# Optimization experiments

Measured on AMD Instinct MI355X. Metric: run time of the kernel, lower is better.

## Reference

```python
import jax, jax.numpy as jnp
import numpy as np

N_NODES = 50000
N_EDGES = 1600000
IN_DIM = 128
HID = 64   # per-head hidden/out dim
HEADS = 2
NEG_SLOPE = 0.2


def _gat_layer(x, src, dst, W, attn_l, attn_r, bias):
    # x: [N, Fin]; W: [Fin, H*D]; attn_l/attn_r: [H, D]; bias: [H, D]
    N = x.shape[0]
    H, D = attn_l.shape
    feat = (x @ W).reshape(N, H, D)                      # [N,H,D]
    el = jnp.sum(feat * attn_l, axis=-1)                 # [N,H]
    er = jnp.sum(feat * attn_r, axis=-1)                 # [N,H]
    e = jax.nn.leaky_relu(el[src] + er[dst], NEG_SLOPE)  # [E,H]
    # segment softmax over destination nodes
    m = jax.ops.segment_max(e, dst, num_segments=N)      # [N,H]
    ex = jnp.exp(e - m[dst])                             # [E,H]
    s = jax.ops.segment_sum(ex, dst, num_segments=N)     # [N,H]
    alpha = ex / s[dst]                                  # [E,H]
    msg = feat[src] * alpha[..., None]                   # [E,H,D]
    out = jax.ops.segment_sum(msg, dst, num_segments=N)  # [N,H,D]
    out = out + bias                                     # per-head bias
    # encoder: mean over heads, then ELU
    return jax.nn.elu(out.mean(axis=1))                  # [N,D]


def setup_inputs() -> dict:
    key = jax.random.key(0)
    ks = jax.random.split(key, 12)
    features = jax.random.normal(ks[0], (N_NODES, IN_DIM), dtype=jnp.float32)
    src = jax.random.randint(ks[1], (N_EDGES,), 0, N_NODES, dtype=jnp.int32)
    dst = jax.random.randint(ks[2], (N_EDGES,), 0, N_NODES, dtype=jnp.int32)
    sc1 = 1.0 / np.sqrt(IN_DIM)
    sc2 = 1.0 / np.sqrt(HID)
    W1 = jax.random.normal(ks[3], (IN_DIM, HEADS * HID), dtype=jnp.float32) * sc1
    al1 = jax.random.normal(ks[4], (HEADS, HID), dtype=jnp.float32) * sc2
    ar1 = jax.random.normal(ks[5], (HEADS, HID), dtype=jnp.float32) * sc2
    b1 = jnp.zeros((HEADS, HID), dtype=jnp.float32)
    W2 = jax.random.normal(ks[6], (HID, HEADS * HID), dtype=jnp.float32) * sc2
    al2 = jax.random.normal(ks[7], (HEADS, HID), dtype=jnp.float32) * sc2
    ar2 = jax.random.normal(ks[8], (HEADS, HID), dtype=jnp.float32) * sc2
    b2 = jnp.zeros((HEADS, HID), dtype=jnp.float32)
    return {"features": features, "W1": W1, "al1": al1, "ar1": ar1, "b1": b1,
            "W2": W2, "al2": al2, "ar2": ar2, "b2": b2, "src": src, "dst": dst}


def reference(features, W1, al1, ar1, b1, W2, al2, ar2, b2, src, dst):
    h = _gat_layer(features, src, dst, W1, al1, ar1, b1)  # [N, HID]
    h = _gat_layer(h, src, dst, W2, al2, ar2, b2)         # [N, HID]
    return h
```

## Files before the change

### kernel.cpp

```cpp
#include <hip/hip_runtime.h>
#include <hip/hip_fp16.h>
#include <math.h>

#define N_NODES 50000
#define N_EDGES 1600000
#define SLOTS 96
#define NODES_PER_GRP 6250
#define FILL_BLOCKS 832
#define GEMM1_BLOCKS ((N_NODES + 31) / 32)

typedef int v4i __attribute__((ext_vector_type(4)));


__global__ __launch_bounds__(256) void fused_fill_gemm1(
    const int* __restrict__ src, const int* __restrict__ dst,
    int* __restrict__ cursor, int* __restrict__ ssrc,
    const float* __restrict__ x,
    const float* __restrict__ W,
    const float* __restrict__ al,
    const float* __restrict__ ar,
    __half* __restrict__ feat,
    float* __restrict__ el,
    float* __restrict__ er) {
    constexpr int K = 128;
    constexpr int LDX = K + 4;
    __shared__ float xs[32 * LDX];

    if (blockIdx.x < FILL_BLOCKS) {
        const int g = blockIdx.x & 7;
        const int bg = blockIdx.x >> 3;
        const int nbg = FILL_BLOCKS >> 3;
        const int lo = g * NODES_PER_GRP;
        const int hi = lo + NODES_PER_GRP;
        const v4i* d4 = (const v4i*)dst;
        const v4i* s4 = (const v4i*)src;
        const int E4 = N_EDGES >> 2;

        for (int i = bg * 256 + threadIdx.x; i < E4; i += nbg * 256) {
            v4i d = __builtin_nontemporal_load(d4 + i);
            v4i s = __builtin_nontemporal_load(s4 + i);
            if (d.x >= lo && d.x < hi) {
                int p = atomicAdd(&cursor[d.x], 1);
                if (p < SLOTS) ssrc[d.x * SLOTS + p] = s.x;
            }
            if (d.y >= lo && d.y < hi) {
                int p = atomicAdd(&cursor[d.y], 1);
                if (p < SLOTS) ssrc[d.y * SLOTS + p] = s.y;
            }
            if (d.z >= lo && d.z < hi) {
                int p = atomicAdd(&cursor[d.z], 1);
                if (p < SLOTS) ssrc[d.z * SLOTS + p] = s.z;
            }
            if (d.w >= lo && d.w < hi) {
                int p = atomicAdd(&cursor[d.w], 1);
                if (p < SLOTS) ssrc[d.w * SLOTS + p] = s.w;
            }
        }
        return;
    }

    const int tid = threadIdx.x;
    const int node0 = (blockIdx.x - FILL_BLOCKS) * 32;
    const int N = N_NODES;

    for (int i = tid; i < 32 * K / 4; i += 256) {
        int r = i / (K / 4), c4 = i % (K / 4);
        float4 v = make_float4(0.f, 0.f, 0.f, 0.f);
        if (node0 + r < N) v = *(const float4*)&x[(size_t)(node0 + r) * K + c4 * 4];
        *(float4*)&xs[r * LDX + c4 * 4] = v;
    }
    __syncthreads();

    const int tx = tid & 31;
    const int ty = tid >> 5;
    const int col = tx * 4;

    float acc[4][4];
#pragma unroll
    for (int r = 0; r < 4; ++r)
#pragma unroll
        for (int c = 0; c < 4; ++c) acc[r][c] = 0.f;

    for (int kb = 0; kb < K / 4; ++kb) {
        float4 w0 = *(const float4*)&W[(kb * 4 + 0) * 128 + col];
        float4 w1 = *(const float4*)&W[(kb * 4 + 1) * 128 + col];
        float4 w2 = *(const float4*)&W[(kb * 4 + 2) * 128 + col];
        float4 w3 = *(const float4*)&W[(kb * 4 + 3) * 128 + col];
        float4 xv[4];
#pragma unroll
        for (int r = 0; r < 4; ++r)
            xv[r] = *(const float4*)&xs[(ty * 4 + r) * LDX + kb * 4];
#pragma unroll
        for (int r = 0; r < 4; ++r) {
            acc[r][0] += xv[r].x * w0.x + xv[r].y * w1.x + xv[r].z * w2.x + xv[r].w * w3.x;
            acc[r][1] += xv[r].x * w0.y + xv[r].y * w1.y + xv[r].z * w2.y + xv[r].w * w3.y;
            acc[r][2] += xv[r].x * w0.z + xv[r].y * w1.z + xv[r].z * w2.z + xv[r].w * w3.z;
            acc[r][3] += xv[r].x * w0.w + xv[r].y * w1.w + xv[r].z * w2.w + xv[r].w * w3.w;
        }
    }

    float4 alv = *(const float4*)&al[col];
    float4 arv = *(const float4*)&ar[col];
    float elp[4], erp[4];
#pragma unroll
    for (int r = 0; r < 4; ++r) {
        int n = node0 + ty * 4 + r;
        float4 f = make_float4(acc[r][0], acc[r][1], acc[r][2], acc[r][3]);
        if (n < N) {
            __half2 p0 = __floats2half2_rn(f.x, f.y);
            __half2 p1 = __floats2half2_rn(f.z, f.w);
            union { __half2 h2[2]; uint2 u; } pk;
            pk.h2[0] = p0; pk.h2[1] = p1;
            *(uint2*)&feat[(size_t)n * 128 + col] = pk.u;
        }
        elp[r] = f.x * alv.x + f.y * alv.y + f.z * alv.z + f.w * alv.w;
        erp[r] = f.x * arv.x + f.y * arv.y + f.z * arv.z + f.w * arv.w;
    }
#pragma unroll
    for (int m = 1; m <= 8; m <<= 1) {
#pragma unroll
        for (int r = 0; r < 4; ++r) {
            elp[r] += __shfl_xor(elp[r], m, 64);
            erp[r] += __shfl_xor(erp[r], m, 64);
        }
    }
    int h = tx >> 4;
    if ((tx & 15) == 0) {
#pragma unroll
        for (int r = 0; r < 4; ++r) {
            int n = node0 + ty * 4 + r;
            if (n < N) {
                el[n * 2 + h] = elp[r];
                er[n * 2 + h] = erp[r];
            }
        }
    }
}


template <int K>
__global__ __launch_bounds__(256) void gemm_elr_kernel(
    const float* __restrict__ x, const float* __restrict__ W,
    const float* __restrict__ al, const float* __restrict__ ar,
    __half* __restrict__ feat, float* __restrict__ el, float* __restrict__ er,
    int N) {
    constexpr int LDX = K + 4;
    __shared__ float xs[32 * LDX];
    const int tid = threadIdx.x;
    const int node0 = blockIdx.x * 32;

    for (int i = tid; i < 32 * K / 4; i += 256) {
        int r = i / (K / 4), c4 = i % (K / 4);
        float4 v = make_float4(0.f, 0.f, 0.f, 0.f);
        if (node0 + r < N) v = *(const float4*)&x[(size_t)(node0 + r) * K + c4 * 4];
        *(float4*)&xs[r * LDX + c4 * 4] = v;
    }
    __syncthreads();

    const int tx = tid & 31;
    const int ty = tid >> 5;
    const int col = tx * 4;

    float acc[4][4];
#pragma unroll
    for (int r = 0; r < 4; ++r)
#pragma unroll
        for (int c = 0; c < 4; ++c) acc[r][c] = 0.f;

    for (int kb = 0; kb < K / 4; ++kb) {
        float4 w0 = *(const float4*)&W[(kb * 4 + 0) * 128 + col];
        float4 w1 = *(const float4*)&W[(kb * 4 + 1) * 128 + col];
        float4 w2 = *(const float4*)&W[(kb * 4 + 2) * 128 + col];
        float4 w3 = *(const float4*)&W[(kb * 4 + 3) * 128 + col];
        float4 xv[4];
#pragma unroll
        for (int r = 0; r < 4; ++r)
            xv[r] = *(const float4*)&xs[(ty * 4 + r) * LDX + kb * 4];
#pragma unroll
        for (int r = 0; r < 4; ++r) {
            acc[r][0] += xv[r].x * w0.x + xv[r].y * w1.x + xv[r].z * w2.x + xv[r].w * w3.x;
            acc[r][1] += xv[r].x * w0.y + xv[r].y * w1.y + xv[r].z * w2.y + xv[r].w * w3.y;
            acc[r][2] += xv[r].x * w0.z + xv[r].y * w1.z + xv[r].z * w2.z + xv[r].w * w3.z;
            acc[r][3] += xv[r].x * w0.w + xv[r].y * w1.w + xv[r].z * w2.w + xv[r].w * w3.w;
        }
    }

    float4 alv = *(const float4*)&al[col];
    float4 arv = *(const float4*)&ar[col];
    float elp[4], erp[4];
#pragma unroll
    for (int r = 0; r < 4; ++r) {
        int n = node0 + ty * 4 + r;
        float4 f = make_float4(acc[r][0], acc[r][1], acc[r][2], acc[r][3]);
        if (n < N) {
            __half2 p0 = __floats2half2_rn(f.x, f.y);
            __half2 p1 = __floats2half2_rn(f.z, f.w);
            union { __half2 h2[2]; uint2 u; } pk;
            pk.h2[0] = p0; pk.h2[1] = p1;
            *(uint2*)&feat[(size_t)n * 128 + col] = pk.u;
        }
        elp[r] = f.x * alv.x + f.y * alv.y + f.z * alv.z + f.w * alv.w;
        erp[r] = f.x * arv.x + f.y * arv.y + f.z * arv.z + f.w * arv.w;
    }
#pragma unroll
    for (int m = 1; m <= 8; m <<= 1) {
#pragma unroll
        for (int r = 0; r < 4; ++r) {
            elp[r] += __shfl_xor(elp[r], m, 64);
            erp[r] += __shfl_xor(erp[r], m, 64);
        }
    }
    int h = tx >> 4;
    if ((tx & 15) == 0) {
#pragma unroll
        for (int r = 0; r < 4; ++r) {
            int n = node0 + ty * 4 + r;
            if (n < N) {
                el[n * 2 + h] = elp[r];
                er[n * 2 + h] = erp[r];
            }
        }
    }
}


__global__ __launch_bounds__(256) void aggregate_kernel(
    const __half* __restrict__ feat, const float* __restrict__ el,
    const float* __restrict__ er, const int* __restrict__ deg,
    const int* __restrict__ ssrc, const float* __restrict__ bias,
    float* __restrict__ hout, int N) {
    const int wave = threadIdx.x >> 6;
    const int lane = threadIdx.x & 63;
    const int n = blockIdx.x * 4 + wave;
    if (n >= N) return;

    const int q = lane >> 3;
    const int ql = lane & 7;
    const int h = ql >> 2;
    const float er_h = er[n * 2 + h];
    const int start = n * SLOTS;
    int d = deg[n];
    if (d > SLOTS) d = SLOTS;

    float acc[16];
#pragma unroll
    for (int j = 0; j < 16; ++j) acc[j] = 0.f;
    float ssum = 0.f;

    for (int base = 0; base < d; base += 8) {
        int idx = base + q;
        bool valid = idx < d;
        int s = ssrc[start + (valid ? idx : 0)];
        float e = el[s * 2 + h] + er_h;
        e = e > 0.f ? e : 0.2f * e;
        float x = valid ? __expf(e) : 0.f;
        const float4* fp = (const float4*)(feat + (size_t)s * 128 + ql * 16);
        float4 ra = fp[0];
        float4 rb = fp[1];
        const __half2* ha = (const __half2*)&ra;
        const __half2* hb = (const __half2*)&rb;
        ssum += x;
#pragma unroll
        for (int j = 0; j < 4; ++j) {
            float2 fa = __half22float2(ha[j]);
            float2 fb = __half22float2(hb[j]);
            acc[j * 2 + 0] += x * fa.x;
            acc[j * 2 + 1] += x * fa.y;
            acc[8 + j * 2 + 0] += x * fb.x;
            acc[8 + j * 2 + 1] += x * fb.y;
        }
    }

#pragma unroll
    for (int m = 8; m <= 32; m <<= 1) {
#pragma unroll
        for (int j = 0; j < 16; ++j) acc[j] += __shfl_xor(acc[j], m, 64);
        ssum += __shfl_xor(ssum, m, 64);
    }

    float inv = (d > 0) ? 1.0f / ssum : 0.0f;
    float v[16];
#pragma unroll
    for (int j = 0; j < 4; ++j) {
        float4 b = *(const float4*)&bias[ql * 16 + j * 4];
        v[j * 4 + 0] = acc[j * 4 + 0] * inv + b.x;
        v[j * 4 + 1] = acc[j * 4 + 1] * inv + b.y;
        v[j * 4 + 2] = acc[j * 4 + 2] * inv + b.z;
        v[j * 4 + 3] = acc[j * 4 + 3] * inv + b.w;
    }

    float o[16];
#pragma unroll
    for (int j = 0; j < 16; ++j) {
        float p = __shfl_xor(v[j], 4, 64);
        float t = 0.5f * (v[j] + p);
        o[j] = t > 0.f ? t : expm1f(t);
    }
    if (lane < 4) {
#pragma unroll
        for (int j = 0; j < 4; ++j) {
            float4 w = make_float4(o[j * 4 + 0], o[j * 4 + 1], o[j * 4 + 2], o[j * 4 + 3]);
            *(float4*)&hout[(size_t)n * 64 + ql * 16 + j * 4] = w;
        }
    }
}


extern "C" void kernel_launch(void* const* d_in, const int* in_sizes, int n_in,
                              void* d_out, int out_size, void* d_ws, size_t ws_size,
                              hipStream_t stream) {
    const float* features = (const float*)d_in[0];
    const float* W1 = (const float*)d_in[1];
    const float* al1 = (const float*)d_in[2];
    const float* ar1 = (const float*)d_in[3];
    const float* b1 = (const float*)d_in[4];
    const float* W2 = (const float*)d_in[5];
    const float* al2 = (const float*)d_in[6];
    const float* ar2 = (const float*)d_in[7];
    const float* b2 = (const float*)d_in[8];
    const int* src = (const int*)d_in[9];
    const int* dst = (const int*)d_in[10];
    float* out = (float*)d_out;

    const int N = N_NODES;

    char* ws = (char*)d_ws;
    size_t off = 0;
    auto alloc = [&](size_t bytes) {
        void* p = ws + off;
        off = (off + bytes + 255) & ~255ULL;
        return p;
    };
    int* cursor   = (int*)alloc((size_t)N * 4);
    int* ssrc     = (int*)alloc((size_t)N * SLOTS * 4);
    __half* feath = (__half*)alloc((size_t)N * 128 * 2);
    float* el     = (float*)alloc((size_t)N * 2 * 4);
    float* er     = (float*)alloc((size_t)N * 2 * 4);
    float* h1     = (float*)alloc((size_t)N * 64 * 4);

    hipMemsetAsync(cursor, 0, (size_t)N * 4, stream);

    fused_fill_gemm1<<<FILL_BLOCKS + GEMM1_BLOCKS, 256, 0, stream>>>(
        src, dst, cursor, ssrc, features, W1, al1, ar1, feath, el, er);

    aggregate_kernel<<<(N + 3) / 4, 256, 0, stream>>>(feath, el, er, cursor, ssrc,
                                                      b1, h1, N);
    gemm_elr_kernel<64><<<(N + 31) / 32, 256, 0, stream>>>(h1, W2, al2, ar2,
                                                           feath, el, er, N);
    aggregate_kernel<<<(N + 3) / 4, 256, 0, stream>>>(feath, el, er, cursor, ssrc,
                                                      b2, out, N);
}
```

Baseline: 390.6 us.

## Fuse layer-1 aggregation with layer-2 GEMM and attention logits per node

Replaces the separate layer-1 aggregate kernel and the tiled layer-2 GEMM with one per-node wave kernel. After the softmax-weighted aggregation, bias, head mean and ELU, each wave multiplies its 64-wide hidden vector by W2 using shuffles and writes fp16 features plus el/er for layer 2. This removes the h1 round trip through global memory and one launch. The trade-off is that W2 is re-read from global/L2 for every node with no shared-memory tiling, and the GEMM becomes a per-wave shuffle loop. Separate el/er and feature buffers are used for the two layers to avoid read/write conflicts.

Result: no change. 392.9 us (+0.6%).

```diff
diff --git a/kernel.cpp b/kernel.cpp
--- a/kernel.cpp
+++ b/kernel.cpp
@@ -138,88 +138,111 @@
 }
 
 
-template <int K>
-__global__ __launch_bounds__(256) void gemm_elr_kernel(
-    const float* __restrict__ x, const float* __restrict__ W,
-    const float* __restrict__ al, const float* __restrict__ ar,
-    __half* __restrict__ feat, float* __restrict__ el, float* __restrict__ er,
+__global__ __launch_bounds__(256) void agg_gemm_kernel(
+    const __half* __restrict__ feat,
+    const float* __restrict__ el,
+    const float* __restrict__ er,
+    const int* __restrict__ deg,
+    const int* __restrict__ ssrc,
+    const float* __restrict__ bias,
+    const float* __restrict__ W2,
+    const float* __restrict__ al2,
+    const float* __restrict__ ar2,
+    __half* __restrict__ feat2,
+    float* __restrict__ el2,
+    float* __restrict__ er2,
     int N) {
-    constexpr int LDX = K + 4;
-    __shared__ float xs[32 * LDX];
-    const int tid = threadIdx.x;
-    const int node0 = blockIdx.x * 32;
-
-    for (int i = tid; i < 32 * K / 4; i += 256) {
-        int r = i / (K / 4), c4 = i % (K / 4);
-        float4 v = make_float4(0.f, 0.f, 0.f, 0.f);
-        if (node0 + r < N) v = *(const float4*)&x[(size_t)(node0 + r) * K + c4 * 4];
-        *(float4*)&xs[r * LDX + c4 * 4] = v;
-    }
-    __syncthreads();
-
-    const int tx = tid & 31;
-    const int ty = tid >> 5;
-    const int col = tx * 4;
-
-    float acc[4][4];
-#pragma unroll
-    for (int r = 0; r < 4; ++r)
-#pragma unroll
-        for (int c = 0; c < 4; ++c) acc[r][c] = 0.f;
-
-    for (int kb = 0; kb < K / 4; ++kb) {
-        float4 w0 = *(const float4*)&W[(kb * 4 + 0) * 128 + col];
-        float4 w1 = *(const float4*)&W[(kb * 4 + 1) * 128 + col];
-        float4 w2 = *(const float4*)&W[(kb * 4 + 2) * 128 + col];
-        float4 w3 = *(const float4*)&W[(kb * 4 + 3) * 128 + col];
-        float4 xv[4];
-#pragma unroll
-        for (int r = 0; r < 4; ++r)
-            xv[r] = *(const float4*)&xs[(ty * 4 + r) * LDX + kb * 4];
-#pragma unroll
-        for (int r = 0; r < 4; ++r) {
-            acc[r][0] += xv[r].x * w0.x + xv[r].y * w1.x + xv[r].z * w2.x + xv[r].w * w3.x;
-            acc[r][1] += xv[r].x * w0.y + xv[r].y * w1.y + xv[r].z * w2.y + xv[r].w * w3.y;
-            acc[r][2] += xv[r].x * w0.z + xv[r].y * w1.z + xv[r].z * w2.z + xv[r].w * w3.z;
-            acc[r][3] += xv[r].x * w0.w + xv[r].y * w1.w + xv[r].z * w2.w + xv[r].w * w3.w;
-        }
-    }
-
-    float4 alv = *(const float4*)&al[col];
-    float4 arv = *(const float4*)&ar[col];
-    float elp[4], erp[4];
-#pragma unroll
-    for (int r = 0; r < 4; ++r) {
-        int n = node0 + ty * 4 + r;
-        float4 f = make_float4(acc[r][0], acc[r][1], acc[r][2], acc[r][3]);
-        if (n < N) {
-            __half2 p0 = __floats2half2_rn(f.x, f.y);
-            __half2 p1 = __floats2half2_rn(f.z, f.w);
-            union { __half2 h2[2]; uint2 u; } pk;
-            pk.h2[0] = p0; pk.h2[1] = p1;
-            *(uint2*)&feat[(size_t)n * 128 + col] = pk.u;
-        }
-        elp[r] = f.x * alv.x + f.y * alv.y + f.z * alv.z + f.w * alv.w;
-        erp[r] = f.x * arv.x + f.y * arv.y + f.z * arv.z + f.w * arv.w;
-    }
-#pragma unroll
-    for (int m = 1; m <= 8; m <<= 1) {
-#pragma unroll
-        for (int r = 0; r < 4; ++r) {
-            elp[r] += __shfl_xor(elp[r], m, 64);
-            erp[r] += __shfl_xor(erp[r], m, 64);
-        }
-    }
-    int h = tx >> 4;
-    if ((tx & 15) == 0) {
-#pragma unroll
-        for (int r = 0; r < 4; ++r) {
-            int n = node0 + ty * 4 + r;
-            if (n < N) {
-                el[n * 2 + h] = elp[r];
-                er[n * 2 + h] = erp[r];
-            }
-        }
+    const int wave = threadIdx.x >> 6;
+    const int lane = threadIdx.x & 63;
+    const int n = blockIdx.x * 4 + wave;
+    if (n >= N) return;
+
+    const int q = lane >> 3;
+    const int ql = lane & 7;
+    const int h = ql >> 2;
+    const float er_h = er[n * 2 + h];
+    const int start = n * SLOTS;
+    int d = deg[n];
+    if (d > SLOTS) d = SLOTS;
+
+    float acc[16];
+#pragma unroll
+    for (int j = 0; j < 16; ++j) acc[j] = 0.f;
+    float ssum = 0.f;
+
+    for (int base = 0; base < d; base += 8) {
+        int idx = base + q;
+        bool valid = idx < d;
+        int s = ssrc[start + (valid ? idx : 0)];
+        float e = el[s * 2 + h] + er_h;
+        e = e > 0.f ? e : 0.2f * e;
+        float x = valid ? __expf(e) : 0.f;
+        const float4* fp = (const float4*)(feat + (size_t)s * 128 + ql * 16);
+        float4 ra = fp[0];
+        float4 rb = fp[1];
+        const __half2* ha = (const __half2*)&ra;
+        const __half2* hb = (const __half2*)&rb;
+        ssum += x;
+#pragma unroll
+        for (int j = 0; j < 4; ++j) {
+            float2 fa = __half22float2(ha[j]);
+            float2 fb = __half22float2(hb[j]);
+            acc[j * 2 + 0] += x * fa.x;
+            acc[j * 2 + 1] += x * fa.y;
+            acc[8 + j * 2 + 0] += x * fb.x;
+            acc[8 + j * 2 + 1] += x * fb.y;
+        }
+    }
+
+#pragma unroll
+    for (int m = 8; m <= 32; m <<= 1) {
+#pragma unroll
+        for (int j = 0; j < 16; ++j) acc[j] += __shfl_xor(acc[j], m, 64);
+        ssum += __shfl_xor(ssum, m, 64);
+    }
+
+    float inv = (d > 0) ? 1.0f / ssum : 0.0f;
+    float v[16];
+#pragma unroll
+    for (int j = 0; j < 4; ++j) {
+        float4 b = *(const float4*)&bias[ql * 16 + j * 4];
+        v[j * 4 + 0] = acc[j * 4 + 0] * inv + b.x;
+        v[j * 4 + 1] = acc[j * 4 + 1] * inv + b.y;
+        v[j * 4 + 2] = acc[j * 4 + 2] * inv + b.z;
+        v[j * 4 + 3] = acc[j * 4 + 3] * inv + b.w;
+    }
+
+    float o[16];
+#pragma unroll
+    for (int j = 0; j < 16; ++j) {
+        float p = __shfl_xor(v[j], 4, 64);
+        float t = 0.5f * (v[j] + p);
+        o[j] = t > 0.f ? t : expm1f(t);
+    }
+
+    const int c0 = lane * 2;
+    float a0 = 0.f, a1 = 0.f;
+#pragma unroll
+    for (int k = 0; k < 64; ++k) {
+        float hk = __shfl(o[k & 15], k >> 4, 64);
+        float2 w = *(const float2*)&W2[k * 128 + c0];
+        a0 += hk * w.x;
+        a1 += hk * w.y;
+    }
+
+    *(__half2*)&feat2[(size_t)n * 128 + c0] = __floats2half2_rn(a0, a1);
+
+    float elp = a0 * al2[c0] + a1 * al2[c0 + 1];
+    float erp = a0 * ar2[c0] + a1 * ar2[c0 + 1];
+#pragma unroll
+    for (int m = 1; m <= 16; m <<= 1) {
+        elp += __shfl_xor(elp, m, 64);
+        erp += __shfl_xor(erp, m, 64);
+    }
+    if ((lane & 31) == 0) {
+        int hh = lane >> 5;
+        el2[n * 2 + hh] = elp;
+        er2[n * 2 + hh] = erp;
     }
 }
 
@@ -331,22 +354,23 @@
         off = (off + bytes + 255) & ~255ULL;
         return p;
     };
-    int* cursor   = (int*)alloc((size_t)N * 4);
-    int* ssrc     = (int*)alloc((size_t)N * SLOTS * 4);
-    __half* feath = (__half*)alloc((size_t)N * 128 * 2);
-    float* el     = (float*)alloc((size_t)N * 2 * 4);
-    float* er     = (float*)alloc((size_t)N * 2 * 4);
-    float* h1     = (float*)alloc((size_t)N * 64 * 4);
+    int* cursor    = (int*)alloc((size_t)N * 4);
+    int* ssrc      = (int*)alloc((size_t)N * SLOTS * 4);
+    __half* feat1h = (__half*)alloc((size_t)N * 128 * 2);
+    __half* feat2h = (__half*)alloc((size_t)N * 128 * 2);
+    float* el1     = (float*)alloc((size_t)N * 2 * 4);
+    float* er1     = (float*)alloc((size_t)N * 2 * 4);
+    float* el2     = (float*)alloc((size_t)N * 2 * 4);
+    float* er2     = (float*)alloc((size_t)N * 2 * 4);
 
     hipMemsetAsync(cursor, 0, (size_t)N * 4, stream);
 
     fused_fill_gemm1<<<FILL_BLOCKS + GEMM1_BLOCKS, 256, 0, stream>>>(
-        src, dst, cursor, ssrc, features, W1, al1, ar1, feath, el, er);
-
-    aggregate_kernel<<<(N + 3) / 4, 256, 0, stream>>>(feath, el, er, cursor, ssrc,
-                                                      b1, h1, N);
-    gemm_elr_kernel<64><<<(N + 31) / 32, 256, 0, stream>>>(h1, W2, al2, ar2,
-                                                           feath, el, er, N);
-    aggregate_kernel<<<(N + 3) / 4, 256, 0, stream>>>(feath, el, er, cursor, ssrc,
-                                                      b2, out, N);
+        src, dst, cursor, ssrc, features, W1, al1, ar1, feat1h, el1, er1);
+
+    agg_gemm_kernel<<<(N + 3) / 4, 256, 0, stream>>>(
+        feat1h, el1, er1, cursor, ssrc, b1, W2, al2, ar2, feat2h, el2, er2, N);
+
+    aggregate_kernel<<<(N + 3) / 4, 256, 0, stream>>>(feat2h, el2, er2, cursor,
+                                                      ssrc, b2, out, N);
 }
```
